# Kernel tuning notes

Hardware: AMD Instinct MI355X
Metric: run time of the kernel (lower is better)

## Reference

```python
import jax, jax.numpy as jnp
import numpy as np

B, N, D = 32, 1024, 256

def setup_inputs() -> dict:
    key = jax.random.key(0)
    ks = jax.random.split(key, 7)
    s = 1.0 / np.sqrt(D)
    return {
        "traj": jax.random.normal(ks[0], (B, N, D), dtype=jnp.float32),
        "Wq": jax.random.normal(ks[1], (D, D), dtype=jnp.float32) * s,
        "bq": jax.random.normal(ks[2], (D,), dtype=jnp.float32) * s,
        "Wk": jax.random.normal(ks[3], (D, D), dtype=jnp.float32) * s,
        "bk": jax.random.normal(ks[4], (D,), dtype=jnp.float32) * s,
        "Wv": jax.random.normal(ks[5], (D, D), dtype=jnp.float32) * s,
        "bv": jax.random.normal(ks[6], (D,), dtype=jnp.float32) * s,
    }

def reference(traj, Wq, bq, Wk, bk, Wv, bv):
    # torch nn.Linear: y = x @ W.T + b
    q = jnp.einsum('bnd,ed->bne', traj, Wq) + bq  # [B,N,D]
    k = jnp.einsum('bnd,ed->bne', traj, Wk) + bk  # [B,N,D]
    v = jnp.einsum('bnd,ed->bne', traj, Wv) + bv  # [B,N,D]
    # unscaled dot-product attention (original sums broadcasted Q*K over D)
    scores = jnp.einsum('bnd,bmd->bnm', q, k)     # [B,N,N]
    attn = jax.nn.softmax(scores, axis=-1)        # [B,N,N]
    out = jnp.einsum('bnm,bmd->bnd', attn, v)     # [B,N,D]
    return out
```

## Files before the change

### kernel.cpp

```cpp
#include <hip/hip_runtime.h>

#define NN 1024
#define DD 256

typedef __attribute__((ext_vector_type(8))) _Float16 f16x8;
typedef __attribute__((ext_vector_type(4))) float f32x4;

union H8 { f16x8 v; _Float16 s[8]; };

__device__ __forceinline__ void g2lds16(const void* g, void* l) {
  __builtin_amdgcn_global_load_lds(
      (const __attribute__((address_space(1))) void*)g,
      (__attribute__((address_space(3))) void*)l, 16, 0, 0);
}

__global__ void wconv_kernel(const float* __restrict__ Wq, const float* __restrict__ Wk,
                             const float* __restrict__ Wv, _Float16* __restrict__ pw) {
  int c = blockIdx.x * 256 + threadIdx.x;
  int lane = c & 63;
  int nt = (c >> 6) & 1;
  int kk = (c >> 7) & 7;
  int et = c >> 10;
  int e = et * 32 + nt * 16 + (lane & 15);
  int d = kk * 32 + (lane >> 4) * 8;
  const float* W = (e < 256) ? Wq : (e < 512 ? Wk : Wv);
  const float* src = W + (e & 255) * 256 + d;
  H8 xx;
  for (int j = 0; j < 8; ++j) xx.s[j] = (_Float16)src[j];
  *(f16x8*)(pw + (size_t)c * 8) = xx.v;
}

__global__ __launch_bounds__(256, 2) void proj_kernel(
    const float* __restrict__ traj,
    const float* __restrict__ bq, const float* __restrict__ bk, const float* __restrict__ bv,
    const _Float16* __restrict__ pw,
    _Float16* __restrict__ pq, _Float16* __restrict__ pk, _Float16* __restrict__ pv)
{
  __shared__ alignas(16) _Float16 Wl[2][8192];
  __shared__ alignas(16) _Float16 Cs[4][1280];

  const int t = threadIdx.x;
  const int lane = t & 63, wave = t >> 6;
  const int col16 = lane & 15, quad = lane >> 4;
  const int mt = blockIdx.x >> 1, eh = blockIdx.x & 1;
  const int mbase = mt * 128;
  const int bb = mbase >> 10;

  f16x8 aq[2][8];
  for (int s = 0; s < 2; ++s) {
    const float* ap = traj + (size_t)(mbase + wave * 32 + s * 16 + col16) * DD;
    for (int kk = 0; kk < 8; ++kk) {
      float4 u0 = *(const float4*)(ap + kk * 32 + quad * 8);
      float4 u1 = *(const float4*)(ap + kk * 32 + quad * 8 + 4);
      H8 xx;
      xx.s[0] = (_Float16)u0.x; xx.s[1] = (_Float16)u0.y;
      xx.s[2] = (_Float16)u0.z; xx.s[3] = (_Float16)u0.w;
      xx.s[4] = (_Float16)u1.x; xx.s[5] = (_Float16)u1.y;
      xx.s[6] = (_Float16)u1.z; xx.s[7] = (_Float16)u1.w;
      aq[s][kk] = xx.v;
    }
  }

  const f32x4 zero = {0.f, 0.f, 0.f, 0.f};
  const int et0 = eh * 12;

  for (int i = 0; i < 4; ++i)
    g2lds16(pw + (size_t)et0 * 8192 + (size_t)(i * 256 + t) * 8, Wl[0] + (i * 256 + t) * 8);

  for (int ei = 0; ei < 12; ++ei) {
    __syncthreads();
    if (ei < 11) {
      const _Float16* ws = pw + (size_t)(et0 + ei + 1) * 8192;
      _Float16* wd = Wl[(ei + 1) & 1];
      for (int i = 0; i < 4; ++i)
        g2lds16(ws + (size_t)(i * 256 + t) * 8, wd + (i * 256 + t) * 8);
    }
    const _Float16* wl = Wl[ei & 1];

    f32x4 acc[2][2];
    acc[0][0] = zero; acc[0][1] = zero; acc[1][0] = zero; acc[1][1] = zero;
    for (int kk = 0; kk < 8; ++kk)
      for (int nt = 0; nt < 2; ++nt) {
        f16x8 bw = *(const f16x8*)&wl[((kk * 2 + nt) * 64 + lane) * 8];
        acc[0][nt] = __builtin_amdgcn_mfma_f32_16x16x32_f16(aq[0][kk], bw, acc[0][nt], 0, 0, 0);
        acc[1][nt] = __builtin_amdgcn_mfma_f32_16x16x32_f16(aq[1][kk], bw, acc[1][nt], 0, 0, 0);
      }

    int e0 = eh * 384 + ei * 32;
    int sel = e0 >> 8;
    const float* bias = (sel == 0) ? bq : (sel == 1 ? bk : bv);
    for (int nt = 0; nt < 2; ++nt) {
      float bvl = bias[(e0 & 255) + nt * 16 + col16];
      for (int s = 0; s < 2; ++s) {
        acc[s][nt][0] += bvl; acc[s][nt][1] += bvl;
        acc[s][nt][2] += bvl; acc[s][nt][3] += bvl;
      }
    }

    _Float16* cs = Cs[wave];
    if (sel < 2) {
      for (int s = 0; s < 2; ++s)
        for (int nt = 0; nt < 2; ++nt)
          for (int r = 0; r < 4; ++r)
            cs[(s * 16 + quad * 4 + r) * 40 + nt * 16 + col16] = (_Float16)acc[s][nt][r];
      if (sel == 0) {
        for (int s = 0; s < 2; ++s) {
          f16x8 val = *(const f16x8*)&cs[(s * 16 + col16) * 40 + quad * 8];
          int g = (mbase >> 4) + wave * 2 + s;
          *(f16x8*)(pq + (size_t)((g * 8 + ei) * 64 + lane) * 8) = val;
        }
      } else {
        int kkg = (e0 - 256) >> 5;
        for (int s = 0; s < 2; ++s) {
          f16x8 val = *(const f16x8*)&cs[(s * 16 + col16) * 40 + quad * 8];
          int kgg = ((mbase & 1023) >> 4) + wave * 2 + s;
          *(f16x8*)(pk + (size_t)(((bb * 64 + kgg) * 8 + kkg) * 64 + lane) * 8) = val;
        }
      }
    } else {
      for (int s = 0; s < 2; ++s)
        for (int nt = 0; nt < 2; ++nt)
          for (int r = 0; r < 4; ++r)
            cs[(nt * 16 + col16) * 40 + s * 16 + quad * 4 + r] = (_Float16)acc[s][nt][r];
      int kt32 = ((mbase & 1023) >> 5) + wave;
      for (int dtl = 0; dtl < 2; ++dtl) {
        f16x8 val = *(const f16x8*)&cs[(dtl * 16 + col16) * 40 + quad * 8];
        int dtg = ((e0 - 512) >> 4) + dtl;
        *(f16x8*)(pv + (size_t)(((bb * 32 + kt32) * 16 + dtg) * 64 + lane) * 8) = val;
      }
    }
  }
}

__global__ __launch_bounds__(256, 3) void attn_kernel(
    const _Float16* __restrict__ pq, const _Float16* __restrict__ pk,
    const _Float16* __restrict__ pv, float* __restrict__ out)
{
  __shared__ alignas(16) _Float16 Ks[2][8192];
  __shared__ alignas(16) _Float16 Vs[8192];

  const int t = threadIdx.x;
  const int lane = t & 63, wave = t >> 6;
  const int col16 = lane & 15, quad = lane >> 4;
  const int b = blockIdx.x, qt = blockIdx.y;
  const int qrow0 = b * NN + qt * 64;

  f16x8 aq[8];
  {
    int g = b * 64 + qt * 4 + wave;
    for (int kk = 0; kk < 8; ++kk)
      aq[kk] = *(const f16x8*)(pq + (size_t)((g * 8 + kk) * 64 + lane) * 8);
  }

  float m_i = -3.0e38f, l_i = 0.f;
  f32x4 O[16];
  const f32x4 zero = {0.f, 0.f, 0.f, 0.f};
  for (int dt = 0; dt < 16; ++dt) O[dt] = zero;

  const _Float16* kbb = pk + (size_t)b * 64 * 8 * 64 * 8;
  const _Float16* vbb = pv + (size_t)b * 32 * 16 * 64 * 8;

  for (int i = 0; i < 4; ++i)
    g2lds16(kbb + (size_t)(i * 256 + t) * 8, Ks[0] + (i * 256 + t) * 8);

  for (int kt = 0; kt < 32; ++kt) {
    __syncthreads();
    {
      const _Float16* vg = vbb + (size_t)kt * 8192;
      for (int i = 0; i < 4; ++i)
        g2lds16(vg + (size_t)(i * 256 + t) * 8, Vs + (i * 256 + t) * 8);
      if (kt < 31) {
        const _Float16* kg = kbb + (size_t)(kt + 1) * 8192;
        _Float16* kd = Ks[(kt + 1) & 1];
        for (int i = 0; i < 4; ++i)
          g2lds16(kg + (size_t)(i * 256 + t) * 8, kd + (i * 256 + t) * 8);
      }
    }

    const _Float16* ks = Ks[kt & 1];
    f32x4 S[2]; S[0] = zero; S[1] = zero;
    for (int kk = 0; kk < 8; ++kk)
      for (int nt = 0; nt < 2; ++nt) {
        f16x8 bk_ = *(const f16x8*)&ks[((nt * 8 + kk) * 64 + lane) * 8];
        S[nt] = __builtin_amdgcn_mfma_f32_16x16x32_f16(aq[kk], bk_, S[nt], 0, 0, 0);
      }

    __syncthreads();

    float* Sp = (float*)Ks[kt & 1];
    for (int nt = 0; nt < 2; ++nt)
      for (int r = 0; r < 4; ++r)
        Sp[(wave * 16 + quad * 4 + r) * 36 + nt * 16 + col16] = S[nt][r];
    float sv[8];
    *(f32x4*)&sv[0] = *(const f32x4*)&Sp[(wave * 16 + col16) * 36 + quad * 8];
    *(f32x4*)&sv[4] = *(const f32x4*)&Sp[(wave * 16 + col16) * 36 + quad * 8 + 4];

    float vmax = sv[0];
    for (int j = 1; j < 8; ++j) vmax = fmaxf(vmax, sv[j]);
    vmax = fmaxf(vmax, __shfl_xor(vmax, 16));
    vmax = fmaxf(vmax, __shfl_xor(vmax, 32));
    float nm = fmaxf(m_i, vmax);
    float alpha = __expf(m_i - nm);
    float rs = 0.f;
    H8 px;
    for (int j = 0; j < 8; ++j) {
      float pj = __expf(sv[j] - nm);
      rs += pj;
      px.s[j] = (_Float16)pj;
    }
    rs += __shfl_xor(rs, 16);
    rs += __shfl_xor(rs, 32);
    l_i = l_i * alpha + rs;
    m_i = nm;
    f16x8 ap = px.v;

    if (__ballot(alpha < 1.0f)) {
      float a4[4];
      for (int r = 0; r < 4; ++r) a4[r] = __shfl(alpha, quad * 4 + r);
      for (int dt = 0; dt < 16; ++dt)
        for (int r = 0; r < 4; ++r) O[dt][r] *= a4[r];
    }

    for (int dt = 0; dt < 16; ++dt) {
      f16x8 bv_ = *(const f16x8*)&Vs[(dt * 64 + lane) * 8];
      O[dt] = __builtin_amdgcn_mfma_f32_16x16x32_f16(ap, bv_, O[dt], 0, 0, 0);
    }
  }

  float linv[4];
  for (int r = 0; r < 4; ++r) linv[r] = 1.0f / __shfl(l_i, quad * 4 + r);
  for (int r = 0; r < 4; ++r) {
    float* orow = out + (size_t)(qrow0 + wave * 16 + quad * 4 + r) * DD;
    for (int dt = 0; dt < 16; ++dt)
      orow[dt * 16 + col16] = O[dt][r] * linv[r];
  }
}

extern "C" void kernel_launch(void* const* d_in, const int* in_sizes, int n_in,
                              void* d_out, int out_size, void* d_ws, size_t ws_size,
                              hipStream_t stream) {
  const float* traj = (const float*)d_in[0];
  const float* Wq   = (const float*)d_in[1];
  const float* bq   = (const float*)d_in[2];
  const float* Wk   = (const float*)d_in[3];
  const float* bk   = (const float*)d_in[4];
  const float* Wv   = (const float*)d_in[5];
  const float* bv   = (const float*)d_in[6];

  _Float16* pq = (_Float16*)d_ws;
  _Float16* pk = pq + (size_t)32768 * 256;
  _Float16* pv = pk + (size_t)32768 * 256;
  _Float16* pw = pv + (size_t)32768 * 256;

  wconv_kernel<<<96, 256, 0, stream>>>(Wq, Wk, Wv, pw);
  proj_kernel<<<512, 256, 0, stream>>>(traj, bq, bk, bv, pw, pq, pk, pv);
  attn_kernel<<<dim3(32, 16), 256, 0, stream>>>(pq, pk, pv, (float*)d_out);
}
```

Before: 171.9 us.

## Double-buffer K/V tiles, drop LDS score transpose, add lazy softmax rescale

The attention kernel now double-buffers both the K and V tiles, issuing loads two tiles ahead and controlling completion with explicit vmcnt waits and raw barriers. Swapping the MFMA operands puts the scores in the register layout the P·V MFMA expects, which removes the shared-memory transpose of S and one barrier per iteration. The online softmax only rescales when the row max grows by more than 8, and the MFMA blocks raise wave priority with setprio. The V-producing kernel's pack layout is changed to match the new P layout. The larger LDS footprint cuts occupancy from 3 to 2 blocks per CU, and the lazy rescale risks fp16 overflow of P if scores grow by less than 8 but exp still becomes large.

```diff
diff --git a/kernel.cpp b/kernel.cpp
--- a/kernel.cpp
+++ b/kernel.cpp
@@ -4,6 +4,7 @@
 #define DD 256
 
 typedef __attribute__((ext_vector_type(8))) _Float16 f16x8;
+typedef __attribute__((ext_vector_type(4))) _Float16 f16x4;
 typedef __attribute__((ext_vector_type(4))) float f32x4;
 
 union H8 { f16x8 v; _Float16 s[8]; };
@@ -124,20 +125,23 @@
             cs[(nt * 16 + col16) * 40 + s * 16 + quad * 4 + r] = (_Float16)acc[s][nt][r];
       int kt32 = ((mbase & 1023) >> 5) + wave;
       for (int dtl = 0; dtl < 2; ++dtl) {
-        f16x8 val = *(const f16x8*)&cs[(dtl * 16 + col16) * 40 + quad * 8];
+        const _Float16* base = &cs[(dtl * 16 + col16) * 40];
+        H8 val;
+        *(f16x4*)&val.s[0] = *(const f16x4*)&base[quad * 4];
+        *(f16x4*)&val.s[4] = *(const f16x4*)&base[16 + quad * 4];
         int dtg = ((e0 - 512) >> 4) + dtl;
-        *(f16x8*)(pv + (size_t)(((bb * 32 + kt32) * 16 + dtg) * 64 + lane) * 8) = val;
-      }
-    }
-  }
-}
-
-__global__ __launch_bounds__(256, 3) void attn_kernel(
+        *(f16x8*)(pv + (size_t)(((bb * 32 + kt32) * 16 + dtg) * 64 + lane) * 8) = val.v;
+      }
+    }
+  }
+}
+
+__global__ __launch_bounds__(256, 2) void attn_kernel(
     const _Float16* __restrict__ pq, const _Float16* __restrict__ pk,
     const _Float16* __restrict__ pv, float* __restrict__ out)
 {
   __shared__ alignas(16) _Float16 Ks[2][8192];
-  __shared__ alignas(16) _Float16 Vs[8192];
+  __shared__ alignas(16) _Float16 Vs[2][8192];
 
   const int t = threadIdx.x;
   const int lane = t & 63, wave = t >> 6;
@@ -148,6 +152,7 @@
   f16x8 aq[8];
   {
     int g = b * 64 + qt * 4 + wave;
+#pragma unroll
     for (int kk = 0; kk < 8; ++kk)
       aq[kk] = *(const f16x8*)(pq + (size_t)((g * 8 + kk) * 64 + lane) * 8);
   }
@@ -155,82 +160,106 @@
   float m_i = -3.0e38f, l_i = 0.f;
   f32x4 O[16];
   const f32x4 zero = {0.f, 0.f, 0.f, 0.f};
+#pragma unroll
   for (int dt = 0; dt < 16; ++dt) O[dt] = zero;
 
   const _Float16* kbb = pk + (size_t)b * 64 * 8 * 64 * 8;
   const _Float16* vbb = pv + (size_t)b * 32 * 16 * 64 * 8;
 
-  for (int i = 0; i < 4; ++i)
-    g2lds16(kbb + (size_t)(i * 256 + t) * 8, Ks[0] + (i * 256 + t) * 8);
+#pragma unroll
+  for (int i = 0; i < 4; ++i) g2lds16(kbb + (size_t)(i * 256 + t) * 8, &Ks[0][(i * 256 + t) * 8]);
+#pragma unroll
+  for (int i = 0; i < 4; ++i) g2lds16(vbb + (size_t)(i * 256 + t) * 8, &Vs[0][(i * 256 + t) * 8]);
+#pragma unroll
+  for (int i = 0; i < 4; ++i) g2lds16(kbb + 8192 + (size_t)(i * 256 + t) * 8, &Ks[1][(i * 256 + t) * 8]);
+#pragma unroll
+  for (int i = 0; i < 4; ++i) g2lds16(vbb + 8192 + (size_t)(i * 256 + t) * 8, &Vs[1][(i * 256 + t) * 8]);
 
   for (int kt = 0; kt < 32; ++kt) {
-    __syncthreads();
-    {
-      const _Float16* vg = vbb + (size_t)kt * 8192;
-      for (int i = 0; i < 4; ++i)
-        g2lds16(vg + (size_t)(i * 256 + t) * 8, Vs + (i * 256 + t) * 8);
-      if (kt < 31) {
-        const _Float16* kg = kbb + (size_t)(kt + 1) * 8192;
-        _Float16* kd = Ks[(kt + 1) & 1];
-        for (int i = 0; i < 4; ++i)
-          g2lds16(kg + (size_t)(i * 256 + t) * 8, kd + (i * 256 + t) * 8);
-      }
-    }
+    if (kt < 31) asm volatile("s_waitcnt vmcnt(8)" ::: "memory");
+    else         asm volatile("s_waitcnt vmcnt(0)" ::: "memory");
+    __builtin_amdgcn_s_barrier();
+    asm volatile("" ::: "memory");
 
     const _Float16* ks = Ks[kt & 1];
     f32x4 S[2]; S[0] = zero; S[1] = zero;
+    __builtin_amdgcn_s_setprio(1);
+#pragma unroll
     for (int kk = 0; kk < 8; ++kk)
+#pragma unroll
       for (int nt = 0; nt < 2; ++nt) {
         f16x8 bk_ = *(const f16x8*)&ks[((nt * 8 + kk) * 64 + lane) * 8];
-        S[nt] = __builtin_amdgcn_mfma_f32_16x16x32_f16(aq[kk], bk_, S[nt], 0, 0, 0);
-      }
-
-    __syncthreads();
-
-    float* Sp = (float*)Ks[kt & 1];
+        S[nt] = __builtin_amdgcn_mfma_f32_16x16x32_f16(bk_, aq[kk], S[nt], 0, 0, 0);
+      }
+    __builtin_amdgcn_s_setprio(0);
+
+    float sv[8];
+#pragma unroll
     for (int nt = 0; nt < 2; ++nt)
-      for (int r = 0; r < 4; ++r)
-        Sp[(wave * 16 + quad * 4 + r) * 36 + nt * 16 + col16] = S[nt][r];
-    float sv[8];
-    *(f32x4*)&sv[0] = *(const f32x4*)&Sp[(wave * 16 + col16) * 36 + quad * 8];
-    *(f32x4*)&sv[4] = *(const f32x4*)&Sp[(wave * 16 + col16) * 36 + quad * 8 + 4];
-
+#pragma unroll
+      for (int r = 0; r < 4; ++r) sv[nt * 4 + r] = S[nt][r];
     float vmax = sv[0];
+#pragma unroll
     for (int j = 1; j < 8; ++j) vmax = fmaxf(vmax, sv[j]);
     vmax = fmaxf(vmax, __shfl_xor(vmax, 16));
     vmax = fmaxf(vmax, __shfl_xor(vmax, 32));
-    float nm = fmaxf(m_i, vmax);
-    float alpha = __expf(m_i - nm);
+
+    if (__ballot(vmax > m_i + 8.0f)) {
+      float nm = fmaxf(m_i, vmax);
+      float alpha = __expf(m_i - nm);
+      float a4[4];
+#pragma unroll
+      for (int r = 0; r < 4; ++r) a4[r] = __shfl(alpha, quad * 4 + r);
+#pragma unroll
+      for (int dt = 0; dt < 16; ++dt)
+#pragma unroll
+        for (int r = 0; r < 4; ++r) O[dt][r] *= a4[r];
+      l_i *= alpha;
+      m_i = nm;
+    }
     float rs = 0.f;
     H8 px;
+#pragma unroll
     for (int j = 0; j < 8; ++j) {
-      float pj = __expf(sv[j] - nm);
+      float pj = __expf(sv[j] - m_i);
       rs += pj;
       px.s[j] = (_Float16)pj;
     }
     rs += __shfl_xor(rs, 16);
     rs += __shfl_xor(rs, 32);
-    l_i = l_i * alpha + rs;
-    m_i = nm;
+    l_i += rs;
     f16x8 ap = px.v;
 
-    if (__ballot(alpha < 1.0f)) {
-      float a4[4];
-      for (int r = 0; r < 4; ++r) a4[r] = __shfl(alpha, quad * 4 + r);
-      for (int dt = 0; dt < 16; ++dt)
-        for (int r = 0; r < 4; ++r) O[dt][r] *= a4[r];
-    }
-
+    const _Float16* vs = Vs[kt & 1];
+    __builtin_amdgcn_s_setprio(1);
+#pragma unroll
     for (int dt = 0; dt < 16; ++dt) {
-      f16x8 bv_ = *(const f16x8*)&Vs[(dt * 64 + lane) * 8];
+      f16x8 bv_ = *(const f16x8*)&vs[(dt * 64 + lane) * 8];
       O[dt] = __builtin_amdgcn_mfma_f32_16x16x32_f16(ap, bv_, O[dt], 0, 0, 0);
     }
+    __builtin_amdgcn_s_setprio(0);
+
+    asm volatile("" ::: "memory");
+    __builtin_amdgcn_s_barrier();
+    if (kt < 30) {
+      const _Float16* kg = kbb + (size_t)(kt + 2) * 8192;
+      const _Float16* vg = vbb + (size_t)(kt + 2) * 8192;
+      _Float16* kd = Ks[kt & 1];
+      _Float16* vd = Vs[kt & 1];
+#pragma unroll
+      for (int i = 0; i < 4; ++i) g2lds16(kg + (size_t)(i * 256 + t) * 8, kd + (i * 256 + t) * 8);
+#pragma unroll
+      for (int i = 0; i < 4; ++i) g2lds16(vg + (size_t)(i * 256 + t) * 8, vd + (i * 256 + t) * 8);
+    }
   }
 
   float linv[4];
+#pragma unroll
   for (int r = 0; r < 4; ++r) linv[r] = 1.0f / __shfl(l_i, quad * 4 + r);
+#pragma unroll
   for (int r = 0; r < 4; ++r) {
     float* orow = out + (size_t)(qrow0 + wave * 16 + quad * 4 + r) * DD;
+#pragma unroll
     for (int dt = 0; dt < 16; ++dt)
       orow[dt * 16 + col16] = O[dt][r] * linv[r];
   }
```

Measured after the change: 164.2 us. 4.5% less time.
